# Performance work log

Measured on AMD Instinct MI355X. Metric: run time of the kernel, lower is better.

The kernel has to match this reference:

```python
import jax, jax.numpy as jnp
import numpy as np

V, E, D, B, C = 100000, 256, 128, 8192, 10  # vocab, embedding_size, context_size, batch, window


def setup_inputs() -> dict:
    key = jax.random.key(0)
    ks = jax.random.split(key, 11)
    s = 0.02
    return {
        "x": jax.random.randint(ks[0], (B,), 0, V),
        "context": jax.random.randint(ks[1], (B, C), 0, V),
        "W_emb": jax.random.normal(ks[2], (V, E), jnp.float32) * s,
        "M_w": jax.random.normal(ks[3], (D, E), jnp.float32) * s,
        "M_b": jnp.zeros((D,), jnp.float32),
        "U_w": jax.random.normal(ks[4], (D, 2 * D), jnp.float32) * s,
        "U_b": jnp.zeros((D,), jnp.float32),
        "W_w": jax.random.normal(ks[5], (D, 2 * D), jnp.float32) * s,
        "W_b": jnp.zeros((D,), jnp.float32),
        "prior_mus": jax.random.normal(ks[6], (V, D), jnp.float32) * s,
        # covariance diagonal must be positive for a valid Gaussian (torch would
        # Cholesky-fail otherwise); sample in [0.1, 1.0)
        "prior_sigmas": jax.random.uniform(ks[7], (V, D), jnp.float32, 0.1, 1.0),
    }


def reference(x, context, W_emb, M_w, M_b, U_w, U_b, W_w, W_b, prior_mus, prior_sigmas):
    emb_x = W_emb[x]                       # [B, E]
    emb_c = W_emb[context]                 # [B, C, E]
    Rw = emb_x @ M_w.T + M_b               # [B, D]  (repeated over C slots below)
    Rc = jnp.einsum('bce,de->bcd', emb_c, M_w) + M_b  # [B, C, D]
    RwC = jnp.broadcast_to(Rw[:, None, :], Rc.shape)   # repeat(len(context), 1)
    h = jax.nn.relu(jnp.concatenate([RwC, Rc], axis=-1)).sum(axis=1)  # [B, 2D]
    mu = h @ U_w.T + U_b                   # posterior mean  [B, D]
    sigma = jax.nn.softplus(h @ W_w.T + W_b)  # posterior cov diag [B, D]
    m0 = prior_mus[x]                      # prior mean      [B, D]
    s0 = prior_sigmas[x]                   # prior cov diag  [B, D]
    # closed-form KL(N(m0, diag(s0)) || N(mu, diag(sigma)))
    d = jnp.float32(D)
    kl = 0.5 * ((s0 / sigma).sum(-1)
                + ((mu - m0) ** 2 / sigma).sum(-1)
                - d
                + jnp.log(sigma).sum(-1) - jnp.log(s0).sum(-1))
    return kl  # [B]
```

## Files before the change

### kernel.cpp

```cpp
#include <hip/hip_runtime.h>
#include <hip/hip_bf16.h>
#include <math.h>


#define CTXN  10
#define DDIM  128
#define WS_M   0
#define WS_UW  32768
#define WS_H   98304

typedef short bf16x8 __attribute__((ext_vector_type(8)));
typedef float f32x4  __attribute__((ext_vector_type(4)));

__device__ __forceinline__ uint2 cvt4(float4 v) {
    union { __hip_bfloat162 h2; unsigned u; } a, b;
    a.h2 = __float22bfloat162_rn(make_float2(v.x, v.y));
    b.h2 = __float22bfloat162_rn(make_float2(v.z, v.w));
    return make_uint2(a.u, b.u);
}

__device__ __forceinline__ float softplusf(float v) {
    return fmaxf(v, 0.0f) + log1pf(expf(-fabsf(v)));
}

__global__ __launch_bounds__(256) void k_cvt(
    const float* __restrict__ M_w, const float* __restrict__ U_w,
    const float* __restrict__ W_w, unsigned short* __restrict__ ws)
{
    int which = blockIdx.x >> 5;
    int i = ((blockIdx.x & 31) << 8) | threadIdx.x;
    const float* src = (which == 0) ? M_w : (which == 1) ? U_w : W_w;
    float4 v = ((const float4*)src)[i];
    *(uint2*)&ws[which * 32768 + i * 4] = cvt4(v);
}

#define BT1   8
#define ROWSP 96
#define LP2   264

__global__ __launch_bounds__(512, 4) void bsg_h(
    const int* __restrict__ x, const int* __restrict__ ctx,
    const float* __restrict__ W_emb, const float* __restrict__ M_b,
    const unsigned short* __restrict__ wsr, unsigned short* __restrict__ hws)
{
    __shared__ __align__(16) unsigned short A_s[ROWSP * LP2];

    const int tid  = threadIdx.x;
    const int b0   = blockIdx.x * BT1;
    const int w    = tid >> 6;
    const int lane = tid & 63;
    const int l15  = lane & 15;
    const int lg   = lane >> 4;

    const int rs = tid >> 6;
    const int qs = tid & 63;
    const int bm = b0 + rs;

    const int xb = x[bm];
    int ci[10];
    {
        const int2* crow = (const int2*)(ctx + (size_t)bm * CTXN);
#pragma unroll
        for (int k = 0; k < 5; ++k) { int2 t = crow[k]; ci[2 * k] = t.x; ci[2 * k + 1] = t.y; }
    }

    const float4* We = (const float4*)W_emb;
    float4 rr[11];
    rr[0] = We[(size_t)xb * 64 + qs];
#pragma unroll
    for (int c = 1; c < 11; ++c) rr[c] = We[(size_t)ci[c - 1] * 64 + qs];
#pragma unroll
    for (int c = 0; c < 11; ++c)
        *(uint2*)&A_s[(8 * c + rs) * LP2 + 4 * qs] = cvt4(rr[c]);
    __syncthreads();

    const unsigned short* Mb_bf = wsr + WS_M;
    const int mrow = 16 * w + l15;
    f32x4 acc[6] = {};
#pragma unroll
    for (int ch = 0; ch < 4; ++ch) {
        bf16x8 m0 = *(const bf16x8*)&Mb_bf[mrow * 256 + 64 * ch + 8 * lg];
        bf16x8 m1 = *(const bf16x8*)&Mb_bf[mrow * 256 + 64 * ch + 32 + 8 * lg];
#pragma unroll
        for (int mt = 0; mt < 6; ++mt) {
            bf16x8 a0 = *(const bf16x8*)&A_s[(16 * mt + l15) * LP2 + 64 * ch + 8 * lg];
            bf16x8 a1 = *(const bf16x8*)&A_s[(16 * mt + l15) * LP2 + 64 * ch + 32 + 8 * lg];
            acc[mt] = __builtin_amdgcn_mfma_f32_16x16x32_bf16(a0, m0, acc[mt], 0, 0, 0);
            acc[mt] = __builtin_amdgcn_mfma_f32_16x16x32_bf16(a1, m1, acc[mt], 0, 0, 0);
        }
    }

    const int dg = 16 * w + l15;
    const float mb = M_b[dg];
    float p1[4] = {0, 0, 0, 0}, p2[4] = {0, 0, 0, 0};
#pragma unroll
    for (int mt = 0; mt < 6; ++mt) {
#pragma unroll
        for (int q = 0; q < 4; ++q) {
            float r = fmaxf(acc[mt][q] + mb, 0.0f);
            if (lg < 2) { if (mt == 0) p1[q] = r; else p2[q] += r; }
            else        { if (mt < 5)  p2[q] += r; }
        }
    }
#pragma unroll
    for (int q = 0; q < 4; ++q) {
        float other = __shfl_xor(p2[q], 32);
        if (lg < 2) {
            int b = 4 * lg + q;
            __hip_bfloat16 t1 = __float2bfloat16(10.0f * p1[q]);
            __hip_bfloat16 t2 = __float2bfloat16(p2[q] + other);
            hws[(size_t)(b0 + b) * 256 + dg]       = *(unsigned short*)&t1;
            hws[(size_t)(b0 + b) * 256 + 128 + dg] = *(unsigned short*)&t2;
        }
    }
}

#define BT2  16
#define HLP  264

__global__ __launch_bounds__(512, 4) void bsg_kl(
    const int* __restrict__ x, const float* __restrict__ U_b,
    const float* __restrict__ W_b, const float* __restrict__ pmu,
    const float* __restrict__ psg, const unsigned short* __restrict__ wsr,
    float* __restrict__ out)
{
    __shared__ __align__(16) unsigned short H_s[BT2 * HLP];
    __shared__ float P_s[BT2 * 8];

    const int tid  = threadIdx.x;
    const int b0   = blockIdx.x * BT2;
    const int w    = tid >> 6;
    const int lane = tid & 63;
    const int l15  = lane & 15;
    const int lg   = lane >> 4;
    const int d    = 16 * w + l15;

    float pm[4], ps[4];
#pragma unroll
    for (int q = 0; q < 4; ++q) {
        int xb = x[b0 + 4 * lg + q];
        pm[q] = pmu[(size_t)xb * DDIM + d];
        ps[q] = psg[(size_t)xb * DDIM + d];
    }

    const unsigned short* hws = wsr + WS_H;
    {
        int r = tid >> 5, q = tid & 31;
        *(uint4*)&H_s[r * HLP + 8 * q] =
            *(const uint4*)&hws[(size_t)(b0 + r) * 256 + 8 * q];
    }
    __syncthreads();

    const unsigned short* UWb = wsr + WS_UW;
    f32x4 acc2[2] = {};
#pragma unroll
    for (int ks = 0; ks < 8; ++ks) {
        bf16x8 hf = *(const bf16x8*)&H_s[l15 * HLP + 32 * ks + 8 * lg];
        bf16x8 bu = *(const bf16x8*)&UWb[d * 256 + 32 * ks + 8 * lg];
        bf16x8 bw = *(const bf16x8*)&UWb[(128 + d) * 256 + 32 * ks + 8 * lg];
        acc2[0] = __builtin_amdgcn_mfma_f32_16x16x32_bf16(hf, bu, acc2[0], 0, 0, 0);
        acc2[1] = __builtin_amdgcn_mfma_f32_16x16x32_bf16(hf, bw, acc2[1], 0, 0, 0);
    }

    const float ub = U_b[d], wb = W_b[d];
#pragma unroll
    for (int q = 0; q < 4; ++q) {
        int rb = 4 * lg + q;
        float mu = acc2[0][q] + ub;
        float sg = softplusf(acc2[1][q] + wb);
        float dm = mu - pm[q];
        float p  = ps[q] / sg + dm * dm / sg + logf(sg) - logf(ps[q]);
        p += __shfl_xor(p, 1);
        p += __shfl_xor(p, 2);
        p += __shfl_xor(p, 4);
        p += __shfl_xor(p, 8);
        if (l15 == 0) P_s[rb * 8 + w] = p;
    }
    __syncthreads();
    if (tid < BT2) {
        float s = 0.0f;
#pragma unroll
        for (int k = 0; k < 8; ++k) s += P_s[tid * 8 + k];
        out[b0 + tid] = 0.5f * (s - (float)DDIM);
    }
}

extern "C" void kernel_launch(void* const* d_in, const int* in_sizes, int n_in,
                              void* d_out, int out_size, void* d_ws, size_t ws_size,
                              hipStream_t stream) {
    const int*   x     = (const int*)  d_in[0];
    const int*   ctx   = (const int*)  d_in[1];
    const float* W_emb = (const float*)d_in[2];
    const float* M_w   = (const float*)d_in[3];
    const float* M_b   = (const float*)d_in[4];
    const float* U_w   = (const float*)d_in[5];
    const float* U_b   = (const float*)d_in[6];
    const float* W_w   = (const float*)d_in[7];
    const float* W_b   = (const float*)d_in[8];
    const float* pmu   = (const float*)d_in[9];
    const float* psg   = (const float*)d_in[10];
    float* out = (float*)d_out;
    unsigned short* ws = (unsigned short*)d_ws;

    k_cvt<<<dim3(96), dim3(256), 0, stream>>>(M_w, U_w, W_w, ws);
    bsg_h<<<dim3(8192 / BT1), dim3(512), 0, stream>>>(x, ctx, W_emb, M_b,
                                                      ws, ws + WS_H);
    bsg_kl<<<dim3(8192 / BT2), dim3(512), 0, stream>>>(x, U_b, W_b, pmu, psg,
                                                       ws, out);
}
```

Baseline: 42.73 us.

## Process two batch tiles per block, prefetching second tile's embeddings during MFMA

Each bsg_h block now handles 16 batch rows as two 8-row tiles. All gather indices are staged in shared memory first. The second tile's embedding rows are loaded into registers while the first tile's MFMAs run, which hides gather latency. This halves the grid and reuses the M weight fragments across both tiles, at the cost of more registers (two accumulator sets plus 11 prefetched float4) and possibly lower occupancy.

```diff
diff --git a/kernel.cpp b/kernel.cpp
--- a/kernel.cpp
+++ b/kernel.cpp
@@ -34,8 +34,7 @@
     *(uint2*)&ws[which * 32768 + i * 4] = cvt4(v);
 }
 
-#define BT1   8
-#define ROWSP 96
+#define BT1   16
 #define LP2   264
 
 __global__ __launch_bounds__(512, 4) void bsg_h(
@@ -43,7 +42,8 @@
     const float* __restrict__ W_emb, const float* __restrict__ M_b,
     const unsigned short* __restrict__ wsr, unsigned short* __restrict__ hws)
 {
-    __shared__ __align__(16) unsigned short A_s[ROWSP * LP2];
+    __shared__ __align__(16) unsigned short A_s[96 * LP2];
+    __shared__ int idx_s[192];
 
     const int tid  = threadIdx.x;
     const int b0   = blockIdx.x * BT1;
@@ -52,31 +52,32 @@
     const int l15  = lane & 15;
     const int lg   = lane >> 4;
 
+    if (tid < 192) {
+        int t = (tid >= 96) ? 1 : 0;
+        int u = tid - 96 * t;
+        int c = u >> 3, b = b0 + 8 * t + (u & 7);
+        idx_s[tid] = (c >= 11) ? 0 : ((c == 0) ? x[b] : ctx[b * CTXN + (c - 1)]);
+    }
+    __syncthreads();
+
     const int rs = tid >> 6;
     const int qs = tid & 63;
-    const int bm = b0 + rs;
-
-    const int xb = x[bm];
-    int ci[10];
-    {
-        const int2* crow = (const int2*)(ctx + (size_t)bm * CTXN);
-#pragma unroll
-        for (int k = 0; k < 5; ++k) { int2 t = crow[k]; ci[2 * k] = t.x; ci[2 * k + 1] = t.y; }
-    }
-
     const float4* We = (const float4*)W_emb;
     float4 rr[11];
-    rr[0] = We[(size_t)xb * 64 + qs];
-#pragma unroll
-    for (int c = 1; c < 11; ++c) rr[c] = We[(size_t)ci[c - 1] * 64 + qs];
+
+#pragma unroll
+    for (int c = 0; c < 11; ++c) rr[c] = We[(size_t)idx_s[8 * c + rs] * 64 + qs];
 #pragma unroll
     for (int c = 0; c < 11; ++c)
         *(uint2*)&A_s[(8 * c + rs) * LP2 + 4 * qs] = cvt4(rr[c]);
     __syncthreads();
 
+#pragma unroll
+    for (int c = 0; c < 11; ++c) rr[c] = We[(size_t)idx_s[96 + 8 * c + rs] * 64 + qs];
+
     const unsigned short* Mb_bf = wsr + WS_M;
     const int mrow = 16 * w + l15;
-    f32x4 acc[6] = {};
+    f32x4 acc0[6] = {}, acc1[6] = {};
 #pragma unroll
     for (int ch = 0; ch < 4; ++ch) {
         bf16x8 m0 = *(const bf16x8*)&Mb_bf[mrow * 256 + 64 * ch + 8 * lg];
@@ -85,32 +86,55 @@
         for (int mt = 0; mt < 6; ++mt) {
             bf16x8 a0 = *(const bf16x8*)&A_s[(16 * mt + l15) * LP2 + 64 * ch + 8 * lg];
             bf16x8 a1 = *(const bf16x8*)&A_s[(16 * mt + l15) * LP2 + 64 * ch + 32 + 8 * lg];
-            acc[mt] = __builtin_amdgcn_mfma_f32_16x16x32_bf16(a0, m0, acc[mt], 0, 0, 0);
-            acc[mt] = __builtin_amdgcn_mfma_f32_16x16x32_bf16(a1, m1, acc[mt], 0, 0, 0);
+            acc0[mt] = __builtin_amdgcn_mfma_f32_16x16x32_bf16(a0, m0, acc0[mt], 0, 0, 0);
+            acc0[mt] = __builtin_amdgcn_mfma_f32_16x16x32_bf16(a1, m1, acc0[mt], 0, 0, 0);
+        }
+    }
+    __syncthreads();
+
+#pragma unroll
+    for (int c = 0; c < 11; ++c)
+        *(uint2*)&A_s[(8 * c + rs) * LP2 + 4 * qs] = cvt4(rr[c]);
+    __syncthreads();
+
+#pragma unroll
+    for (int ch = 0; ch < 4; ++ch) {
+        bf16x8 m0 = *(const bf16x8*)&Mb_bf[mrow * 256 + 64 * ch + 8 * lg];
+        bf16x8 m1 = *(const bf16x8*)&Mb_bf[mrow * 256 + 64 * ch + 32 + 8 * lg];
+#pragma unroll
+        for (int mt = 0; mt < 6; ++mt) {
+            bf16x8 a0 = *(const bf16x8*)&A_s[(16 * mt + l15) * LP2 + 64 * ch + 8 * lg];
+            bf16x8 a1 = *(const bf16x8*)&A_s[(16 * mt + l15) * LP2 + 64 * ch + 32 + 8 * lg];
+            acc1[mt] = __builtin_amdgcn_mfma_f32_16x16x32_bf16(a0, m0, acc1[mt], 0, 0, 0);
+            acc1[mt] = __builtin_amdgcn_mfma_f32_16x16x32_bf16(a1, m1, acc1[mt], 0, 0, 0);
         }
     }
 
     const int dg = 16 * w + l15;
     const float mb = M_b[dg];
-    float p1[4] = {0, 0, 0, 0}, p2[4] = {0, 0, 0, 0};
-#pragma unroll
-    for (int mt = 0; mt < 6; ++mt) {
+#pragma unroll
+    for (int t = 0; t < 2; ++t) {
+        const f32x4* acc = t ? acc1 : acc0;
+        float p1[4] = {0, 0, 0, 0}, p2[4] = {0, 0, 0, 0};
+#pragma unroll
+        for (int mt = 0; mt < 6; ++mt) {
+#pragma unroll
+            for (int q = 0; q < 4; ++q) {
+                float r = fmaxf(acc[mt][q] + mb, 0.0f);
+                if (lg < 2) { if (mt == 0) p1[q] = r; else p2[q] += r; }
+                else        { if (mt < 5)  p2[q] += r; }
+            }
+        }
 #pragma unroll
         for (int q = 0; q < 4; ++q) {
-            float r = fmaxf(acc[mt][q] + mb, 0.0f);
-            if (lg < 2) { if (mt == 0) p1[q] = r; else p2[q] += r; }
-            else        { if (mt < 5)  p2[q] += r; }
-        }
-    }
-#pragma unroll
-    for (int q = 0; q < 4; ++q) {
-        float other = __shfl_xor(p2[q], 32);
-        if (lg < 2) {
-            int b = 4 * lg + q;
-            __hip_bfloat16 t1 = __float2bfloat16(10.0f * p1[q]);
-            __hip_bfloat16 t2 = __float2bfloat16(p2[q] + other);
-            hws[(size_t)(b0 + b) * 256 + dg]       = *(unsigned short*)&t1;
-            hws[(size_t)(b0 + b) * 256 + 128 + dg] = *(unsigned short*)&t2;
+            float other = __shfl_xor(p2[q], 32);
+            if (lg < 2) {
+                int b = 8 * t + 4 * lg + q;
+                __hip_bfloat16 t1 = __float2bfloat16(10.0f * p1[q]);
+                __hip_bfloat16 t2 = __float2bfloat16(p2[q] + other);
+                hws[(size_t)(b0 + b) * 256 + dg]       = *(unsigned short*)&t1;
+                hws[(size_t)(b0 + b) * 256 + 128 + dg] = *(unsigned short*)&t2;
+            }
         }
     }
 }
```

Result: no change. 42.04 us (-1.6%).
